# Performance work log

Measured on AMD Instinct MI355X. Metric: run time of the kernel, lower is better.

## Reference

```python
import jax, jax.numpy as jnp
import numpy as np

N_VERTICES = 1_000_000
N_DIM = 128
BATCH = 16384
N_NEG = 10


def setup_inputs() -> dict:
    key = jax.random.key(0)
    k1, k2, k3, k4, k5, k6 = jax.random.split(key, 6)
    pos_v = jax.random.randint(k1, (BATCH,), 0, N_VERTICES)
    pos_u = jax.random.randint(k2, (BATCH,), 0, N_VERTICES)
    neg = jax.random.randint(k3, (BATCH, N_NEG), 0, N_VERTICES)
    weights = jax.random.uniform(k4, (BATCH,), dtype=jnp.float32)
    # learned parameters: two embedding tables (nn.Embedding default init ~ N(0,1))
    emb = jax.random.normal(k5, (N_VERTICES, N_DIM), dtype=jnp.float32)
    emb_ctx = jax.random.normal(k6, (N_VERTICES, N_DIM), dtype=jnp.float32)
    return {"pos_v": pos_v, "pos_u": pos_u, "neg": neg, "weights": weights,
            "emb": emb, "emb_ctx": emb_ctx}


def _proximity(emb_v, emb_u, emb_neg_u, weights):
    # emb_v, emb_u: [B, D]; emb_neg_u: [B, K, D]; weights: [B]
    pos_score = jnp.sum(emb_u * emb_v, axis=1)                      # [B]
    neg_score = jnp.einsum('bkd,bd->bk', emb_neg_u, emb_v)          # [B, K]
    neg_score = jnp.sum(jax.nn.log_sigmoid(-neg_score), axis=1)     # [B]
    return weights * (-jax.nn.log_sigmoid(pos_score) - neg_score)   # [B]


def reference(pos_v, pos_u, neg, weights, emb, emb_ctx):
    emb_v = emb[pos_v]            # [B, D] (shared by both branches)
    emb_neg = emb_ctx[neg]        # [B, K, D] (shared by both branches)
    # first proximity: target-target positive pair
    score_1 = _proximity(emb_v, emb[pos_u], emb_neg, weights)
    # second proximity: target-context positive pair
    score_2 = _proximity(emb_v, emb_ctx[pos_u], emb_neg, weights)
    return score_1, score_2
```

## Files before the change

kernel.cpp:

```cpp
#include <hip/hip_runtime.h>

#define BATCH 16384
#define N_NEG 10
#define N_DIM 128

__device__ __forceinline__ float log_sigmoid(float x) {
    return fminf(x, 0.0f) - log1pf(__expf(-fabsf(x)));
}

__global__ __launch_bounds__(256) void all2vec_kernel(
    const int*   __restrict__ pos_v,
    const int*   __restrict__ pos_u,
    const int*   __restrict__ neg,
    const float* __restrict__ weights,
    const float* __restrict__ emb,
    const float* __restrict__ emb_ctx,
    float*       __restrict__ out)
{
    const int wave = threadIdx.x >> 6;
    const int lane = threadIdx.x & 63;
    const int b = blockIdx.x * 4 + wave;
    if (b >= BATCH) return;

    const float2* e2 = (const float2*)emb;
    const float2* c2 = (const float2*)emb_ctx;

    const long long iv = pos_v[b];
    const long long iu = pos_u[b];

    const float2 v = e2[iv * 64 + lane];

    float acc[12];
    {
        const float2 a = e2[iu * 64 + lane];
        acc[0] = a.x * v.x + a.y * v.y;
        const float2 c = c2[iu * 64 + lane];
        acc[1] = c.x * v.x + c.y * v.y;
    }
#pragma unroll
    for (int k = 0; k < N_NEG; ++k) {
        const long long nk = neg[b * N_NEG + k];
        const float2 n = c2[nk * 64 + lane];
        acc[2 + k] = n.x * v.x + n.y * v.y;
    }

#pragma unroll
    for (int j = 0; j < 12; ++j) {
#pragma unroll
        for (int off = 32; off > 0; off >>= 1)
            acc[j] += __shfl_down(acc[j], off, 64);
    }

    if (lane == 0) {
        const float w = weights[b];
        float negsum = 0.0f;
#pragma unroll
        for (int k = 0; k < N_NEG; ++k)
            negsum += log_sigmoid(-acc[2 + k]);
        out[b]         = w * (-log_sigmoid(acc[0]) - negsum);
        out[BATCH + b] = w * (-log_sigmoid(acc[1]) - negsum);
    }
}

extern "C" void kernel_launch(void* const* d_in, const int* in_sizes, int n_in,
                              void* d_out, int out_size, void* d_ws, size_t ws_size,
                              hipStream_t stream) {
    const int*   pos_v   = (const int*)d_in[0];
    const int*   pos_u   = (const int*)d_in[1];
    const int*   neg     = (const int*)d_in[2];
    const float* weights = (const float*)d_in[3];
    const float* emb     = (const float*)d_in[4];
    const float* emb_ctx = (const float*)d_in[5];
    float*       out     = (float*)d_out;

    const int waves_total = BATCH;
    const int blocks = waves_total / 4;
    all2vec_kernel<<<blocks, 256, 0, stream>>>(pos_v, pos_u, neg, weights,
                                               emb, emb_ctx, out);
}
```

Before: 774.6 us.

## Process two batch rows per wave with float4 gathers and hoisted loads

Each 64-lane wave now handles two batch elements, with 32 lanes per row. Every lane gathers float4 instead of float2, and each butterfly reduction drops from six shuffle steps to five. The negative indices and all row gathers are issued before any arithmetic, which raises memory-level parallelism for these random-access gathers. In exchange the grid is halved and per-thread register use grows from holding ten float4 rows at once.

```diff
diff --git a/kernel.cpp b/kernel.cpp
--- a/kernel.cpp
+++ b/kernel.cpp
@@ -17,41 +17,45 @@
     const float* __restrict__ emb_ctx,
     float*       __restrict__ out)
 {
-    const int wave = threadIdx.x >> 6;
     const int lane = threadIdx.x & 63;
-    const int b = blockIdx.x * 4 + wave;
-    if (b >= BATCH) return;
+    const int waveInBlock = threadIdx.x >> 6;
+    const int half = lane >> 5;
+    const int sub  = lane & 31;
+    const int wgid = blockIdx.x * 4 + waveInBlock;
+    const int b    = wgid * 2 + half;
 
-    const float2* e2 = (const float2*)emb;
-    const float2* c2 = (const float2*)emb_ctx;
+    const float4* e4 = (const float4*)emb;
+    const float4* c4 = (const float4*)emb_ctx;
 
     const long long iv = pos_v[b];
     const long long iu = pos_u[b];
+    int nidx[N_NEG];
+#pragma unroll
+    for (int k = 0; k < N_NEG; ++k) nidx[k] = neg[b * N_NEG + k];
 
-    const float2 v = e2[iv * 64 + lane];
+    const float4 v  = e4[iv * 32 + sub];
+    const float4 ru = e4[iu * 32 + sub];
+    const float4 rc = c4[iu * 32 + sub];
+    float4 rn[N_NEG];
+#pragma unroll
+    for (int k = 0; k < N_NEG; ++k)
+        rn[k] = c4[(long long)nidx[k] * 32 + sub];
 
     float acc[12];
-    {
-        const float2 a = e2[iu * 64 + lane];
-        acc[0] = a.x * v.x + a.y * v.y;
-        const float2 c = c2[iu * 64 + lane];
-        acc[1] = c.x * v.x + c.y * v.y;
-    }
+    acc[0] = ru.x * v.x + ru.y * v.y + ru.z * v.z + ru.w * v.w;
+    acc[1] = rc.x * v.x + rc.y * v.y + rc.z * v.z + rc.w * v.w;
 #pragma unroll
-    for (int k = 0; k < N_NEG; ++k) {
-        const long long nk = neg[b * N_NEG + k];
-        const float2 n = c2[nk * 64 + lane];
-        acc[2 + k] = n.x * v.x + n.y * v.y;
-    }
+    for (int k = 0; k < N_NEG; ++k)
+        acc[2 + k] = rn[k].x * v.x + rn[k].y * v.y + rn[k].z * v.z + rn[k].w * v.w;
 
 #pragma unroll
     for (int j = 0; j < 12; ++j) {
 #pragma unroll
-        for (int off = 32; off > 0; off >>= 1)
-            acc[j] += __shfl_down(acc[j], off, 64);
+        for (int m = 16; m > 0; m >>= 1)
+            acc[j] += __shfl_xor(acc[j], m, 64);
     }
 
-    if (lane == 0) {
+    if (sub == 0) {
         const float w = weights[b];
         float negsum = 0.0f;
 #pragma unroll
@@ -73,7 +77,7 @@
     const float* emb_ctx = (const float*)d_in[5];
     float*       out     = (float*)d_out;
 
-    const int waves_total = BATCH;
+    const int waves_total = BATCH / 2;
     const int blocks = waves_total / 4;
     all2vec_kernel<<<blocks, 256, 0, stream>>>(pos_v, pos_u, neg, weights,
                                                emb, emb_ctx, out);
```

Result: no change. 774.4 us (-0.0%).
